# Kernel tuning notes

Measured on AMD Instinct MI355X. Metric: run time of the kernel, lower is better.

## Reference

```python
import jax, jax.numpy as jnp
import numpy as np

N, E, T = 6144, 98304, 32
D_IN, D, D_FF, H, OUT = 128, 256, 256, 4, 2
DH = D // H
EPS = 1e-5


def setup_inputs() -> dict:
    key = jax.random.key(0)
    ks = jax.random.split(key, 24)
    s = 0.05
    inp = {
        "x": jax.random.normal(ks[0], (N, D_IN), jnp.float32),
        "edge_index": jax.random.randint(ks[1], (2, E), 0, N, jnp.int64 if jax.config.jax_enable_x64 else jnp.int32),
        "timesteps": jnp.sort(jax.random.randint(ks[2], (N,), 0, T)),
        "lin_l_w": jax.random.normal(ks[3], (D, D_IN), jnp.float32) * s,
        "lin_l_b": jnp.zeros((D,), jnp.float32),
        "lin_r_w": jax.random.normal(ks[4], (D, D_IN), jnp.float32) * s,
        "bn_gamma": jnp.ones((D,), jnp.float32),
        "bn_beta": jnp.zeros((D,), jnp.float32),
        "in_proj_w": jax.random.normal(ks[5], (2, 3 * D, D), jnp.float32) * s,
        "in_proj_b": jnp.zeros((2, 3 * D), jnp.float32),
        "out_w": jax.random.normal(ks[6], (2, D, D), jnp.float32) * s,
        "out_b": jnp.zeros((2, D), jnp.float32),
        "ff1_w": jax.random.normal(ks[7], (2, D_FF, D), jnp.float32) * s,
        "ff1_b": jnp.zeros((2, D_FF), jnp.float32),
        "ff2_w": jax.random.normal(ks[8], (2, D, D_FF), jnp.float32) * s,
        "ff2_b": jnp.zeros((2, D), jnp.float32),
        "ln1_g": jnp.ones((2, D), jnp.float32),
        "ln1_b": jnp.zeros((2, D), jnp.float32),
        "ln2_g": jnp.ones((2, D), jnp.float32),
        "ln2_b": jnp.zeros((2, D), jnp.float32),
        "cls_w": jax.random.normal(ks[9], (OUT, D), jnp.float32) * s,
        "cls_b": jnp.zeros((OUT,), jnp.float32),
    }
    return inp


def _layernorm(h, g, b):
    mu = jnp.mean(h, -1, keepdims=True)
    v = jnp.var(h, -1, keepdims=True)
    return (h - mu) * jax.lax.rsqrt(v + EPS) * g + b


def _forward(x, edge_index, timesteps, lin_l_w, lin_l_b, lin_r_w, bn_gamma, bn_beta,
             in_proj_w, in_proj_b, out_w, out_b, ff1_w, ff1_b, ff2_w, ff2_b,
             ln1_g, ln1_b, ln2_g, ln2_b, cls_w, cls_b):
    # SAGEConv (mean aggregation): out = lin_l(mean_{j->i} x_j) + lin_r(x_i)
    src, dst = edge_index[0], edge_index[1]
    agg = jax.ops.segment_sum(x[src], dst, num_segments=N)
    cnt = jax.ops.segment_sum(jnp.ones((E,), x.dtype), dst, num_segments=N)
    agg = agg / jnp.maximum(cnt, 1.0)[:, None]
    h = agg @ lin_l_w.T + lin_l_b + x @ lin_r_w.T

    # BatchNorm1d (training batch stats) + ReLU
    mu = jnp.mean(h, 0)
    var = jnp.var(h, 0)
    h = (h - mu) * jax.lax.rsqrt(var + EPS) * bn_gamma + bn_beta
    h = jax.nn.relu(h)

    # Per-timestep transformer == full attention with block-diagonal mask
    mask = timesteps[:, None] == timesteps[None, :]  # [N, N]
    neg = jnp.finfo(h.dtype).min

    for l in range(2):
        # self-attention (post-norm TransformerEncoderLayer)
        qkv = h @ in_proj_w[l].T + in_proj_b[l]             # [N, 3D]
        q, k, v = jnp.split(qkv, 3, axis=-1)
        q = q.reshape(N, H, DH).transpose(1, 0, 2)          # [H, N, DH]
        k = k.reshape(N, H, DH).transpose(1, 0, 2)
        v = v.reshape(N, H, DH).transpose(1, 0, 2)
        scores = jnp.einsum('hnd,hmd->hnm', q, k) / jnp.sqrt(jnp.asarray(DH, h.dtype))
        scores = jnp.where(mask[None], scores, neg)
        attn = jax.nn.softmax(scores, axis=-1)
        o = jnp.einsum('hnm,hmd->hnd', attn, v).transpose(1, 0, 2).reshape(N, D)
        o = o @ out_w[l].T + out_b[l]
        h = _layernorm(h + o, ln1_g[l], ln1_b[l])
        # FFN
        f = jax.nn.relu(h @ ff1_w[l].T + ff1_b[l]) @ ff2_w[l].T + ff2_b[l]
        h = _layernorm(h + f, ln2_g[l], ln2_b[l])

    return h @ cls_w.T + cls_b  # [N, OUT]


def reference(x, edge_index, timesteps, lin_l_w, lin_l_b, lin_r_w, bn_gamma, bn_beta,
              in_proj_w, in_proj_b, out_w, out_b, ff1_w, ff1_b, ff2_w, ff2_b,
              ln1_g, ln1_b, ln2_g, ln2_b, cls_w, cls_b):
    return _forward(x, edge_index, timesteps, lin_l_w, lin_l_b, lin_r_w, bn_gamma, bn_beta,
                    in_proj_w, in_proj_b, out_w, out_b, ff1_w, ff1_b, ff2_w, ff2_b,
                    ln1_g, ln1_b, ln2_g, ln2_b, cls_w, cls_b)
```

## Files before the change

kernel.cpp:

```cpp
#include <hip/hip_runtime.h>

#define NN   6144
#define EE   98304
#define DIN  128
#define DD   256
#define TT   32
#define NH   4
#define ATTN_Z 6
#define WROWS 3328

typedef __attribute__((ext_vector_type(8))) short short8;
typedef __attribute__((ext_vector_type(4))) float f32x4;
typedef unsigned short u16;

__device__ __forceinline__ float bf2f(u16 u) {
    return __uint_as_float(((unsigned)u) << 16);
}
__device__ __forceinline__ u16 f2bf(float f) {
    unsigned u = __float_as_uint(f);
    return (u16)((u + 0x7fffu + ((u >> 16) & 1u)) >> 16);
}
__device__ __forceinline__ unsigned pk2(float a, float b) {
    return (unsigned)f2bf(a) | ((unsigned)f2bf(b) << 16);
}

__global__ void aml_hist_k(const int* __restrict__ ei, int* __restrict__ deg) {
    int e = blockIdx.x * 256 + threadIdx.x;
    if (e < EE) atomicAdd(&deg[ei[EE + e]], 1);
}

__global__ void aml_scan_k(const int* __restrict__ deg, int* __restrict__ rowptr,
                           int* __restrict__ cursor) {
    int t = threadIdx.x;
    int base = t * 24;
    int loc[24];
    int s = 0;
    #pragma unroll
    for (int j = 0; j < 24; ++j) { loc[j] = s; s += deg[base + j]; }
    __shared__ int part[256];
    part[t] = s;
    __syncthreads();
    for (int o = 1; o < 256; o <<= 1) {
        int v = (t >= o) ? part[t - o] : 0;
        __syncthreads();
        part[t] += v;
        __syncthreads();
    }
    int off = (t > 0) ? part[t - 1] : 0;
    #pragma unroll
    for (int j = 0; j < 24; ++j) {
        rowptr[base + j] = off + loc[j];
        cursor[base + j] = off + loc[j];
    }
    if (t == 255) rowptr[NN] = part[255];
}

__global__ void aml_scatter2_k(const int* __restrict__ ei, int* __restrict__ cursor,
                               int* __restrict__ eid) {
    int e = blockIdx.x * 256 + threadIdx.x;
    if (e >= EE) return;
    int slot = atomicAdd(&cursor[ei[EE + e]], 1);
    eid[slot] = ei[e];
}

__global__ void aml_gather_k(const float* __restrict__ x, const int* __restrict__ rowptr,
                             const int* __restrict__ eid, u16* __restrict__ ac) {
    int node = blockIdx.x * 4 + (threadIdx.x >> 6);
    int lane = threadIdx.x & 63;
    int p0 = rowptr[node], p1 = rowptr[node + 1];
    float ax = 0.f, ay = 0.f;
    int j = p0;
    for (; j + 1 < p1; j += 2) {
        int s0 = eid[j], s1 = eid[j + 1];
        float2 v0 = *(const float2*)(x + (size_t)s0 * DIN + lane * 2);
        float2 v1 = *(const float2*)(x + (size_t)s1 * DIN + lane * 2);
        ax += v0.x + v1.x; ay += v0.y + v1.y;
    }
    if (j < p1) {
        float2 v = *(const float2*)(x + (size_t)eid[j] * DIN + lane * 2);
        ax += v.x; ay += v.y;
    }
    float inv = 1.0f / fmaxf((float)(p1 - p0), 1.0f);
    float2 xr = *(const float2*)(x + (size_t)node * DIN + lane * 2);
    *(unsigned*)(ac + (size_t)node * DD + lane * 2) = pk2(ax * inv, ay * inv);
    *(unsigned*)(ac + (size_t)node * DD + DIN + lane * 2) = pk2(xr.x, xr.y);
}

__global__ void aml_prep_k(const float* __restrict__ lin_l_w, const float* __restrict__ lin_r_w,
                           const float* __restrict__ inp_w, const float* __restrict__ out_w,
                           const float* __restrict__ ff1_w, const float* __restrict__ ff2_w,
                           const int* __restrict__ ts, u16* __restrict__ wb,
                           int* __restrict__ offs) {
    int r = blockIdx.x;
    if (r == WROWS) {
        int t = threadIdx.x;
        if (t <= TT) {
            int lo = 0, hi = NN;
            while (lo < hi) { int mid = (lo + hi) >> 1; if (ts[mid] < t) lo = mid + 1; else hi = mid; }
            offs[t] = lo;
        }
        return;
    }
    int k = threadIdx.x;
    float v;
    if (r < 256) {
        v = (k < DIN) ? lin_l_w[r * DIN + k] : lin_r_w[r * DIN + (k - DIN)];
    } else {
        int r2 = r - 256;
        int l = r2 / 1536, r3 = r2 % 1536;
        const float* src; int rr;
        if (r3 < 768)       { src = inp_w + (size_t)l * 768 * DD; rr = r3; }
        else if (r3 < 1024) { src = out_w + (size_t)l * DD * DD;  rr = r3 - 768; }
        else if (r3 < 1280) { src = ff1_w + (size_t)l * DD * DD;  rr = r3 - 1024; }
        else                { src = ff2_w + (size_t)l * DD * DD;  rr = r3 - 1280; }
        v = src[(size_t)rr * DD + k];
    }
    wb[(size_t)r * DD + k] = f2bf(v);
}

template <int RELU, int AF32, int CF32, int BNSTAT>
__global__ __launch_bounds__(256)
void aml_gemm_k(const void* __restrict__ A, const u16* __restrict__ Wb,
                const float* __restrict__ bias, void* __restrict__ C, int M,
                float* __restrict__ stats) {
    __shared__ __align__(16) unsigned char lds[65536];
    const int t = threadIdx.x;
    const int brow = blockIdx.x * 64;
    const int bcol = blockIdx.y * 64;

    const u16* srcW = Wb + (size_t)bcol * 256;
    #pragma unroll
    for (int p = 0; p < 8; ++p) {
        int c = t + p * 256;
        int row = c >> 5;
        int colb = (c & 31) * 16;
        int dst = row * 512 + (colb ^ ((row & 7) << 4));
        if (AF32) {
            const float* sA = (const float*)A + (size_t)(brow + row) * 256 + (c & 31) * 8;
            float4 a0 = *(const float4*)sA;
            float4 a1 = *(const float4*)(sA + 4);
            uint4 pa = { pk2(a0.x, a0.y), pk2(a0.z, a0.w), pk2(a1.x, a1.y), pk2(a1.z, a1.w) };
            *(uint4*)(lds + dst) = pa;
        } else {
            const u16* sA = (const u16*)A + (size_t)(brow + row) * 256 + (c & 31) * 8;
            *(uint4*)(lds + dst) = *(const uint4*)sA;
        }
        *(uint4*)(lds + 32768 + dst) = *(const uint4*)(srcW + (size_t)row * 256 + (c & 31) * 8);
    }
    __syncthreads();

    const int wave = t >> 6, lane = t & 63;
    const int lrow = lane & 15, lk = lane >> 4;
    const int arow = wave * 16 + lrow;
    f32x4 acc[4] = {};
    #pragma unroll
    for (int ks = 0; ks < 8; ++ks) {
        int kbyte = ks * 64 + lk * 16;
        short8 af = *(const short8*)(lds + arow * 512 + (kbyte ^ ((arow & 7) << 4)));
        #pragma unroll
        for (int ct = 0; ct < 4; ++ct) {
            int wrow = ct * 16 + lrow;
            short8 bf = *(const short8*)(lds + 32768 + wrow * 512 + (kbyte ^ ((wrow & 7) << 4)));
            acc[ct] = __builtin_amdgcn_mfma_f32_16x16x32_bf16(af, bf, acc[ct], 0, 0, 0);
        }
    }

    #pragma unroll
    for (int ct = 0; ct < 4; ++ct) {
        int col = bcol + ct * 16 + lrow;
        float bv = bias[col];
        float s = 0.f, q = 0.f;
        #pragma unroll
        for (int r = 0; r < 4; ++r) {
            int grow = brow + wave * 16 + lk * 4 + r;
            float v = acc[ct][r] + bv;
            if (RELU) v = fmaxf(v, 0.0f);
            if (CF32) ((float*)C)[(size_t)grow * M + col] = v;
            else      ((u16*)C)[(size_t)grow * M + col] = f2bf(v);
            if (BNSTAT) { s += v; q += v * v; }
        }
        if (BNSTAT) {
            s += __shfl_xor(s, 16); s += __shfl_xor(s, 32);
            q += __shfl_xor(q, 16); q += __shfl_xor(q, 32);
            if (lk == 0) {
                atomicAdd(&stats[col], s);
                atomicAdd(&stats[DD + col], q);
            }
        }
    }
}

__global__ void aml_bn_apply_k(float* __restrict__ h, const float* __restrict__ stats,
                               const float* __restrict__ g, const float* __restrict__ b) {
    int idx = blockIdx.x * 256 + threadIdx.x;
    int d = idx & (DD - 1);
    float mu = stats[d] * (1.0f / NN);
    float var = stats[DD + d] * (1.0f / NN) - mu * mu;
    float v = (h[idx] - mu) * rsqrtf(var + 1e-5f) * g[d] + b[d];
    h[idx] = fmaxf(v, 0.0f);
}

template <int CLS>
__global__ __launch_bounds__(256)
void aml_mega_k(const u16* __restrict__ A, const u16* __restrict__ Wb,
                const float* __restrict__ bias, float* __restrict__ h,
                const float* __restrict__ g, const float* __restrict__ bv,
                const float* __restrict__ cls_w, const float* __restrict__ cls_b,
                float* __restrict__ out) {
    __shared__ __align__(16) unsigned char lds[65536];
    const int t = threadIdx.x;
    const int brow = blockIdx.x * 64;

    #pragma unroll
    for (int p = 0; p < 8; ++p) {
        int c = t + p * 256;
        int row = c >> 5;
        int colb = (c & 31) * 16;
        int dst = row * 512 + (colb ^ ((row & 7) << 4));
        const u16* sA = A + (size_t)(brow + row) * 256 + (c & 31) * 8;
        *(uint4*)(lds + dst) = *(const uint4*)sA;
    }
    #pragma unroll
    for (int p = 0; p < 8; ++p) {
        int c = t + p * 256;
        int row = c >> 5;
        int colb = (c & 31) * 16;
        int dst = 32768 + row * 512 + (colb ^ ((row & 7) << 4));
        *(uint4*)(lds + dst) = *(const uint4*)(Wb + (size_t)row * 256 + (c & 31) * 8);
    }
    __syncthreads();

    const int wave = t >> 6, lane = t & 63;
    const int lrow = lane & 15, lk = lane >> 4;
    const int arow = wave * 16 + lrow;

    short8 af[8];
    #pragma unroll
    for (int ks = 0; ks < 8; ++ks) {
        int kbyte = ks * 64 + lk * 16;
        af[ks] = *(const short8*)(lds + arow * 512 + (kbyte ^ ((arow & 7) << 4)));
    }

    f32x4 acc[4][4] = {};
    for (int cT = 0; cT < 4; ++cT) {
        if (cT) {
            __syncthreads();
            #pragma unroll
            for (int p = 0; p < 8; ++p) {
                int c = t + p * 256;
                int row = c >> 5;
                int colb = (c & 31) * 16;
                int dst = 32768 + row * 512 + (colb ^ ((row & 7) << 4));
                *(uint4*)(lds + dst) = *(const uint4*)(Wb + (size_t)(cT * 64 + row) * 256 + (c & 31) * 8);
            }
            __syncthreads();
        }
        #pragma unroll
        for (int ks = 0; ks < 8; ++ks) {
            int kbyte = ks * 64 + lk * 16;
            #pragma unroll
            for (int ct = 0; ct < 4; ++ct) {
                int wrow = ct * 16 + lrow;
                short8 bf = *(const short8*)(lds + 32768 + wrow * 512 + (kbyte ^ ((wrow & 7) << 4)));
                acc[cT][ct] = __builtin_amdgcn_mfma_f32_16x16x32_bf16(af[ks], bf, acc[cT][ct], 0, 0, 0);
            }
        }
    }

    float s[4] = {}, q[4] = {};
    #pragma unroll
    for (int cT = 0; cT < 4; ++cT) {
        #pragma unroll
        for (int ct = 0; ct < 4; ++ct) {
            int col = cT * 64 + ct * 16 + lrow;
            float bvv = bias[col];
            #pragma unroll
            for (int r = 0; r < 4; ++r) {
                int grow = brow + wave * 16 + lk * 4 + r;
                float v = acc[cT][ct][r] + bvv + h[(size_t)grow * DD + col];
                acc[cT][ct][r] = v;
                s[r] += v; q[r] += v * v;
            }
        }
    }
    #pragma unroll
    for (int off = 1; off < 16; off <<= 1) {
        #pragma unroll
        for (int r = 0; r < 4; ++r) {
            s[r] += __shfl_xor(s[r], off);
            q[r] += __shfl_xor(q[r], off);
        }
    }
    float mu[4], iv[4];
    #pragma unroll
    for (int r = 0; r < 4; ++r) {
        mu[r] = s[r] * (1.0f / DD);
        iv[r] = rsqrtf(q[r] * (1.0f / DD) - mu[r] * mu[r] + 1e-5f);
    }
    float c0[4] = {}, c1[4] = {};
    #pragma unroll
    for (int cT = 0; cT < 4; ++cT) {
        #pragma unroll
        for (int ct = 0; ct < 4; ++ct) {
            int col = cT * 64 + ct * 16 + lrow;
            float gv = g[col], bb = bv[col];
            float w0 = CLS ? cls_w[col] : 0.f;
            float w1 = CLS ? cls_w[DD + col] : 0.f;
            #pragma unroll
            for (int r = 0; r < 4; ++r) {
                int grow = brow + wave * 16 + lk * 4 + r;
                float v = (acc[cT][ct][r] - mu[r]) * iv[r] * gv + bb;
                h[(size_t)grow * DD + col] = v;
                if (CLS) { c0[r] += v * w0; c1[r] += v * w1; }
            }
        }
    }
    if (CLS) {
        #pragma unroll
        for (int off = 1; off < 16; off <<= 1) {
            #pragma unroll
            for (int r = 0; r < 4; ++r) {
                c0[r] += __shfl_xor(c0[r], off);
                c1[r] += __shfl_xor(c1[r], off);
            }
        }
        if (lrow == 0) {
            float cb0 = cls_b[0], cb1 = cls_b[1];
            #pragma unroll
            for (int r = 0; r < 4; ++r) {
                int grow = brow + wave * 16 + lk * 4 + r;
                out[grow * 2]     = c0[r] + cb0;
                out[grow * 2 + 1] = c1[r] + cb1;
            }
        }
    }
}

__global__ __launch_bounds__(256)
void aml_attn_k(const u16* __restrict__ qkv, const int* __restrict__ offs,
                u16* __restrict__ o) {
    int tb = blockIdx.x, head = blockIdx.y, z = blockIdx.z;
    int start = offs[tb], end = offs[tb + 1];
    int S = end - start;
    if (S <= z * 64) return;
    int t = threadIdx.x, wave = t >> 6, lane = t & 63;
    int lq = lane & 15, lk = lane >> 4;
    int qoff = head * 64;

    __shared__ __align__(16) unsigned char Kl[8192];
    __shared__ __align__(16) unsigned char Vt[8192];
    __shared__ __align__(16) unsigned char Pl[4][2048];
    __shared__ float Ol[4][16][65];

    int qi = start + z * 64 + wave * 16 + lq;
    int qic = min(qi, end - 1);
    const u16* qp = qkv + (size_t)qic * 768 + qoff + lk * 8;
    short8 qf[2];
    qf[0] = *(const short8*)qp;
    qf[1] = *(const short8*)(qp + 32);

    float m = -1e30f, l = 0.f;
    f32x4 acc[4] = {};

    int ntile = (S + 63) >> 6;
    for (int tile = 0; tile < ntile; ++tile) {
        int jcnt = S - tile * 64; if (jcnt > 64) jcnt = 64;
        {
            int j = t >> 2, d0 = (t & 3) * 16;
            unsigned char* krow = Kl + j * 128;
            if (j < jcnt) {
                const u16* kp = qkv + (size_t)(start + tile * 64 + j) * 768 + 256 + qoff + d0;
                *(uint4*)(krow + ((d0 * 2) ^ ((j & 7) << 4))) = *(const uint4*)kp;
                *(uint4*)(krow + ((d0 * 2 + 16) ^ ((j & 7) << 4))) = *(const uint4*)(kp + 8);
                const u16* vp = kp + 256;
                #pragma unroll
                for (int i = 0; i < 16; ++i) {
                    int d = d0 + i;
                    *(u16*)(Vt + d * 128 + ((j * 2) ^ ((d & 7) << 4))) = vp[i];
                }
            } else {
                uint4 zz = { 0, 0, 0, 0 };
                *(uint4*)(krow + ((d0 * 2) ^ ((j & 7) << 4))) = zz;
                *(uint4*)(krow + ((d0 * 2 + 16) ^ ((j & 7) << 4))) = zz;
                #pragma unroll
                for (int i = 0; i < 16; ++i) {
                    int d = d0 + i;
                    *(u16*)(Vt + d * 128 + ((j * 2) ^ ((d & 7) << 4))) = 0;
                }
            }
        }
        __syncthreads();

        f32x4 sv[4];
        #pragma unroll
        for (int kt = 0; kt < 4; ++kt) {
            int kr = kt * 16 + lq;
            f32x4 s = {};
            #pragma unroll
            for (int ks = 0; ks < 2; ++ks) {
                short8 kf = *(const short8*)(Kl + kr * 128 + ((ks * 64 + lk * 16) ^ ((kr & 7) << 4)));
                s = __builtin_amdgcn_mfma_f32_16x16x32_bf16(kf, qf[ks], s, 0, 0, 0);
            }
            sv[kt] = s;
        }
        float pm = -1e30f;
        #pragma unroll
        for (int kt = 0; kt < 4; ++kt) {
            #pragma unroll
            for (int r = 0; r < 4; ++r) {
                int kk = tile * 64 + kt * 16 + lk * 4 + r;
                float s = (kk < S) ? sv[kt][r] * 0.125f : -1e30f;
                sv[kt][r] = s;
                pm = fmaxf(pm, s);
            }
        }
        pm = fmaxf(pm, __shfl_xor(pm, 16));
        pm = fmaxf(pm, __shfl_xor(pm, 32));
        float mn = fmaxf(m, pm);
        float corr = __expf(m - mn);
        m = mn;
        float ps = 0.f;
        #pragma unroll
        for (int kt = 0; kt < 4; ++kt) {
            #pragma unroll
            for (int r = 0; r < 4; ++r) {
                float p = __expf(sv[kt][r] - mn);
                sv[kt][r] = p;
                ps += p;
            }
            uint2 w = { pk2(sv[kt][0], sv[kt][1]), pk2(sv[kt][2], sv[kt][3]) };
            *(uint2*)(Pl[wave] + lq * 128 + ((kt * 32 + lk * 8) ^ ((lq & 7) << 4))) = w;
        }
        ps += __shfl_xor(ps, 16);
        ps += __shfl_xor(ps, 32);
        l = l * corr + ps;
        #pragma unroll
        for (int dt = 0; dt < 4; ++dt) {
            #pragma unroll
            for (int r = 0; r < 4; ++r) acc[dt][r] *= corr;
        }
        #pragma unroll
        for (int ks = 0; ks < 2; ++ks) {
            short8 pf = *(const short8*)(Pl[wave] + lq * 128 + ((ks * 64 + lk * 16) ^ ((lq & 7) << 4)));
            #pragma unroll
            for (int dt = 0; dt < 4; ++dt) {
                int dr = dt * 16 + lq;
                short8 vf = *(const short8*)(Vt + dr * 128 + ((ks * 64 + lk * 16) ^ ((dr & 7) << 4)));
                acc[dt] = __builtin_amdgcn_mfma_f32_16x16x32_bf16(vf, pf, acc[dt], 0, 0, 0);
            }
        }
        __syncthreads();
    }

    float linv = 1.0f / l;
    #pragma unroll
    for (int dt = 0; dt < 4; ++dt) {
        #pragma unroll
        for (int r = 0; r < 4; ++r)
            Ol[wave][lq][dt * 16 + lk * 4 + r] = acc[dt][r] * linv;
    }
    int q2 = lane >> 2, c2 = lane & 3;
    int qg = start + z * 64 + wave * 16 + q2;
    if (qg < end) {
        u16* op = o + (size_t)qg * DD + qoff + c2 * 16;
        const float* sp = &Ol[wave][q2][c2 * 16];
        #pragma unroll
        for (int i = 0; i < 8; ++i)
            ((unsigned*)op)[i] = pk2(sp[2 * i], sp[2 * i + 1]);
    }
}

extern "C" void kernel_launch(void* const* d_in, const int* in_sizes, int n_in,
                              void* d_out, int out_size, void* d_ws, size_t ws_size,
                              hipStream_t stream) {
    const float* x       = (const float*)d_in[0];
    const int*   ei      = (const int*)d_in[1];
    const int*   ts      = (const int*)d_in[2];
    const float* lin_l_w = (const float*)d_in[3];
    const float* lin_l_b = (const float*)d_in[4];
    const float* lin_r_w = (const float*)d_in[5];
    const float* bn_g    = (const float*)d_in[6];
    const float* bn_b    = (const float*)d_in[7];
    const float* inp_w   = (const float*)d_in[8];
    const float* inp_b   = (const float*)d_in[9];
    const float* out_w   = (const float*)d_in[10];
    const float* out_b   = (const float*)d_in[11];
    const float* ff1_w   = (const float*)d_in[12];
    const float* ff1_b   = (const float*)d_in[13];
    const float* ff2_w   = (const float*)d_in[14];
    const float* ff2_b   = (const float*)d_in[15];
    const float* ln1_g   = (const float*)d_in[16];
    const float* ln1_b   = (const float*)d_in[17];
    const float* ln2_g   = (const float*)d_in[18];
    const float* ln2_b   = (const float*)d_in[19];
    const float* cls_w   = (const float*)d_in[20];
    const float* cls_b   = (const float*)d_in[21];

    float* ws     = (float*)d_ws;
    float* stats  = ws;
    int*   deg    = (int*)(stats + 512);
    int*   rowptr = deg + NN;
    int*   cursor = rowptr + NN + 4;
    int*   eid    = cursor + NN;
    int*   offs   = eid + EE;
    u16*   wb     = (u16*)(offs + 64);
    float* h      = (float*)(wb + (size_t)WROWS * 256);
    u16*   qkv    = (u16*)(h + (size_t)NN * DD);
    u16*   t1     = qkv + (size_t)NN * 768;
    u16*   ac     = qkv;

    const u16* wb_cat = wb;
    const u16* wb_inp[2] = { wb + (size_t)(256) * 256,        wb + (size_t)(256 + 1536) * 256 };
    const u16* wb_out[2] = { wb + (size_t)(256 + 768) * 256,  wb + (size_t)(256 + 1536 + 768) * 256 };
    const u16* wb_ff1[2] = { wb + (size_t)(256 + 1024) * 256, wb + (size_t)(256 + 1536 + 1024) * 256 };
    const u16* wb_ff2[2] = { wb + (size_t)(256 + 1280) * 256, wb + (size_t)(256 + 1536 + 1280) * 256 };

    hipMemsetAsync(stats, 0, 512 * sizeof(float) + NN * sizeof(int), stream);

    aml_hist_k<<<EE / 256, 256, 0, stream>>>(ei, deg);
    aml_scan_k<<<1, 256, 0, stream>>>(deg, rowptr, cursor);
    aml_scatter2_k<<<EE / 256, 256, 0, stream>>>(ei, cursor, eid);
    aml_gather_k<<<NN / 4, 256, 0, stream>>>(x, rowptr, eid, ac);
    aml_prep_k<<<WROWS + 1, 256, 0, stream>>>(lin_l_w, lin_r_w, inp_w, out_w, ff1_w, ff2_w,
                                              ts, wb, offs);
    aml_gemm_k<0, 0, 1, 1><<<dim3(NN / 64, 4), 256, 0, stream>>>(ac, wb_cat, lin_l_b, h, DD, stats);
    aml_bn_apply_k<<<(NN * DD) / 256, 256, 0, stream>>>(h, stats, bn_g, bn_b);

    for (int l = 0; l < 2; ++l) {
        aml_gemm_k<0, 1, 0, 0><<<dim3(NN / 64, 12), 256, 0, stream>>>(h, wb_inp[l],
                                                                      inp_b + (size_t)l * 768,
                                                                      qkv, 768, nullptr);
        aml_attn_k<<<dim3(TT, NH, ATTN_Z), 256, 0, stream>>>(qkv, offs, t1);
        aml_mega_k<0><<<NN / 64, 256, 0, stream>>>(t1, wb_out[l], out_b + (size_t)l * DD, h,
                                                   ln1_g + (size_t)l * DD, ln1_b + (size_t)l * DD,
                                                   nullptr, nullptr, nullptr);
        aml_gemm_k<1, 1, 0, 0><<<dim3(NN / 64, 4), 256, 0, stream>>>(h, wb_ff1[l],
                                                                     ff1_b + (size_t)l * DD,
                                                                     t1, DD, nullptr);
        if (l == 0)
            aml_mega_k<0><<<NN / 64, 256, 0, stream>>>(t1, wb_ff2[l], ff2_b + (size_t)l * DD, h,
                                                       ln2_g + (size_t)l * DD, ln2_b + (size_t)l * DD,
                                                       nullptr, nullptr, nullptr);
        else
            aml_mega_k<1><<<NN / 64, 256, 0, stream>>>(t1, wb_ff2[l], ff2_b + (size_t)l * DD, h,
                                                       ln2_g + (size_t)l * DD, ln2_b + (size_t)l * DD,
                                                       cls_w, cls_b, (float*)d_out);
    }
}
```

Measured before the change: 164.6 us.

## Process two query chunks per attention block to reuse staged K/V tiles

Each attention block now covers 128 queries as two 64-query chunks instead of 64, halving the grid z dimension and reusing each staged K/V tile and K fragments across both chunks. The V transpose into LDS is rewritten to use vectorized 16-byte global loads with packed 32-bit LDS stores instead of scalar u16 traffic. The PV MFMA operand order is swapped so the output is laid out query-per-column, which removes the Ol LDS staging buffer but makes the final stores scattered 2-byte writes and requires shuffles for the per-row correction factors. Fewer blocks and higher register use may reduce parallelism for short timestep segments.

```diff
diff --git a/kernel.cpp b/kernel.cpp
--- a/kernel.cpp
+++ b/kernel.cpp
@@ -6,7 +6,7 @@
 #define DD   256
 #define TT   32
 #define NH   4
-#define ATTN_Z 6
+#define ATTN_Z 3
 #define WROWS 3328
 
 typedef __attribute__((ext_vector_type(8))) short short8;
@@ -342,7 +342,7 @@
     int tb = blockIdx.x, head = blockIdx.y, z = blockIdx.z;
     int start = offs[tb], end = offs[tb + 1];
     int S = end - start;
-    if (S <= z * 64) return;
+    if (S <= z * 128) return;
     int t = threadIdx.x, wave = t >> 6, lane = t & 63;
     int lq = lane & 15, lk = lane >> 4;
     int qoff = head * 64;
@@ -350,17 +350,19 @@
     __shared__ __align__(16) unsigned char Kl[8192];
     __shared__ __align__(16) unsigned char Vt[8192];
     __shared__ __align__(16) unsigned char Pl[4][2048];
-    __shared__ float Ol[4][16][65];
-
-    int qi = start + z * 64 + wave * 16 + lq;
-    int qic = min(qi, end - 1);
-    const u16* qp = qkv + (size_t)qic * 768 + qoff + lk * 8;
-    short8 qf[2];
-    qf[0] = *(const short8*)qp;
-    qf[1] = *(const short8*)(qp + 32);
-
-    float m = -1e30f, l = 0.f;
-    f32x4 acc[4] = {};
+
+    short8 qf[2][2];
+    float m[2], l[2];
+    f32x4 acc[2][4] = {};
+    #pragma unroll
+    for (int c = 0; c < 2; ++c) {
+        int qi = start + z * 128 + c * 64 + wave * 16 + lq;
+        int qic = min(qi, end - 1);
+        const u16* qp = qkv + (size_t)qic * 768 + qoff + lk * 8;
+        qf[c][0] = *(const short8*)qp;
+        qf[c][1] = *(const short8*)(qp + 32);
+        m[c] = -1e30f; l[c] = 0.f;
+    }
 
     int ntile = (S + 63) >> 6;
     for (int tile = 0; tile < ntile; ++tile) {
@@ -372,101 +374,115 @@
                 const u16* kp = qkv + (size_t)(start + tile * 64 + j) * 768 + 256 + qoff + d0;
                 *(uint4*)(krow + ((d0 * 2) ^ ((j & 7) << 4))) = *(const uint4*)kp;
                 *(uint4*)(krow + ((d0 * 2 + 16) ^ ((j & 7) << 4))) = *(const uint4*)(kp + 8);
-                const u16* vp = kp + 256;
-                #pragma unroll
-                for (int i = 0; i < 16; ++i) {
-                    int d = d0 + i;
-                    *(u16*)(Vt + d * 128 + ((j * 2) ^ ((d & 7) << 4))) = vp[i];
-                }
             } else {
                 uint4 zz = { 0, 0, 0, 0 };
                 *(uint4*)(krow + ((d0 * 2) ^ ((j & 7) << 4))) = zz;
                 *(uint4*)(krow + ((d0 * 2 + 16) ^ ((j & 7) << 4))) = zz;
-                #pragma unroll
-                for (int i = 0; i < 16; ++i) {
-                    int d = d0 + i;
-                    *(u16*)(Vt + d * 128 + ((j * 2) ^ ((d & 7) << 4))) = 0;
-                }
+            }
+        }
+        {
+            int j0 = (t & 31) * 2, d0v = (t >> 5) * 8;
+            const u16* vbase = qkv + (size_t)(start + tile * 64) * 768 + 512 + qoff + d0v;
+            uint4 va = { 0, 0, 0, 0 }, vb = { 0, 0, 0, 0 };
+            if (j0 < jcnt)     va = *(const uint4*)(vbase + (size_t)j0 * 768);
+            if (j0 + 1 < jcnt) vb = *(const uint4*)(vbase + (size_t)(j0 + 1) * 768);
+            const u16* pa = (const u16*)&va;
+            const u16* pb = (const u16*)&vb;
+            #pragma unroll
+            for (int i = 0; i < 8; ++i) {
+                int d = d0v + i;
+                unsigned w = (unsigned)pa[i] | ((unsigned)pb[i] << 16);
+                *(unsigned*)(Vt + d * 128 + ((j0 * 2) ^ ((d & 7) << 4))) = w;
             }
         }
         __syncthreads();
 
-        f32x4 sv[4];
+        short8 kf[4][2];
         #pragma unroll
         for (int kt = 0; kt < 4; ++kt) {
             int kr = kt * 16 + lq;
-            f32x4 s = {};
+            #pragma unroll
+            for (int ks = 0; ks < 2; ++ks)
+                kf[kt][ks] = *(const short8*)(Kl + kr * 128 + ((ks * 64 + lk * 16) ^ ((kr & 7) << 4)));
+        }
+
+        #pragma unroll
+        for (int c = 0; c < 2; ++c) {
+            if (z * 128 + c * 64 >= S) break;
+            f32x4 sv[4];
+            #pragma unroll
+            for (int kt = 0; kt < 4; ++kt) {
+                f32x4 s = {};
+                s = __builtin_amdgcn_mfma_f32_16x16x32_bf16(kf[kt][0], qf[c][0], s, 0, 0, 0);
+                s = __builtin_amdgcn_mfma_f32_16x16x32_bf16(kf[kt][1], qf[c][1], s, 0, 0, 0);
+                sv[kt] = s;
+            }
+            float pm = -1e30f;
+            #pragma unroll
+            for (int kt = 0; kt < 4; ++kt) {
+                #pragma unroll
+                for (int r = 0; r < 4; ++r) {
+                    int kk = tile * 64 + kt * 16 + lk * 4 + r;
+                    float s = (kk < S) ? sv[kt][r] * 0.125f : -1e30f;
+                    sv[kt][r] = s;
+                    pm = fmaxf(pm, s);
+                }
+            }
+            pm = fmaxf(pm, __shfl_xor(pm, 16));
+            pm = fmaxf(pm, __shfl_xor(pm, 32));
+            float mn = fmaxf(m[c], pm);
+            float corr = __expf(m[c] - mn);
+            m[c] = mn;
+            float ps = 0.f;
+            #pragma unroll
+            for (int kt = 0; kt < 4; ++kt) {
+                #pragma unroll
+                for (int r = 0; r < 4; ++r) {
+                    float p = __expf(sv[kt][r] - mn);
+                    sv[kt][r] = p;
+                    ps += p;
+                }
+                uint2 w = { pk2(sv[kt][0], sv[kt][1]), pk2(sv[kt][2], sv[kt][3]) };
+                *(uint2*)(Pl[wave] + lq * 128 + ((kt * 32 + lk * 8) ^ ((lq & 7) << 4))) = w;
+            }
+            ps += __shfl_xor(ps, 16);
+            ps += __shfl_xor(ps, 32);
+            l[c] = l[c] * corr + ps;
+            float cr[4];
+            #pragma unroll
+            for (int r = 0; r < 4; ++r) cr[r] = __shfl(corr, lk * 4 + r);
+            #pragma unroll
+            for (int dt = 0; dt < 4; ++dt)
+                #pragma unroll
+                for (int r = 0; r < 4; ++r) acc[c][dt][r] *= cr[r];
             #pragma unroll
             for (int ks = 0; ks < 2; ++ks) {
-                short8 kf = *(const short8*)(Kl + kr * 128 + ((ks * 64 + lk * 16) ^ ((kr & 7) << 4)));
-                s = __builtin_amdgcn_mfma_f32_16x16x32_bf16(kf, qf[ks], s, 0, 0, 0);
-            }
-            sv[kt] = s;
-        }
-        float pm = -1e30f;
-        #pragma unroll
-        for (int kt = 0; kt < 4; ++kt) {
-            #pragma unroll
-            for (int r = 0; r < 4; ++r) {
-                int kk = tile * 64 + kt * 16 + lk * 4 + r;
-                float s = (kk < S) ? sv[kt][r] * 0.125f : -1e30f;
-                sv[kt][r] = s;
-                pm = fmaxf(pm, s);
-            }
-        }
-        pm = fmaxf(pm, __shfl_xor(pm, 16));
-        pm = fmaxf(pm, __shfl_xor(pm, 32));
-        float mn = fmaxf(m, pm);
-        float corr = __expf(m - mn);
-        m = mn;
-        float ps = 0.f;
-        #pragma unroll
-        for (int kt = 0; kt < 4; ++kt) {
-            #pragma unroll
-            for (int r = 0; r < 4; ++r) {
-                float p = __expf(sv[kt][r] - mn);
-                sv[kt][r] = p;
-                ps += p;
-            }
-            uint2 w = { pk2(sv[kt][0], sv[kt][1]), pk2(sv[kt][2], sv[kt][3]) };
-            *(uint2*)(Pl[wave] + lq * 128 + ((kt * 32 + lk * 8) ^ ((lq & 7) << 4))) = w;
-        }
-        ps += __shfl_xor(ps, 16);
-        ps += __shfl_xor(ps, 32);
-        l = l * corr + ps;
-        #pragma unroll
-        for (int dt = 0; dt < 4; ++dt) {
-            #pragma unroll
-            for (int r = 0; r < 4; ++r) acc[dt][r] *= corr;
-        }
-        #pragma unroll
-        for (int ks = 0; ks < 2; ++ks) {
-            short8 pf = *(const short8*)(Pl[wave] + lq * 128 + ((ks * 64 + lk * 16) ^ ((lq & 7) << 4)));
-            #pragma unroll
-            for (int dt = 0; dt < 4; ++dt) {
-                int dr = dt * 16 + lq;
-                short8 vf = *(const short8*)(Vt + dr * 128 + ((ks * 64 + lk * 16) ^ ((dr & 7) << 4)));
-                acc[dt] = __builtin_amdgcn_mfma_f32_16x16x32_bf16(vf, pf, acc[dt], 0, 0, 0);
+                short8 pf = *(const short8*)(Pl[wave] + lq * 128 + ((ks * 64 + lk * 16) ^ ((lq & 7) << 4)));
+                #pragma unroll
+                for (int dt = 0; dt < 4; ++dt) {
+                    int dr = dt * 16 + lq;
+                    short8 vf = *(const short8*)(Vt + dr * 128 + ((ks * 64 + lk * 16) ^ ((dr & 7) << 4)));
+                    acc[c][dt] = __builtin_amdgcn_mfma_f32_16x16x32_bf16(pf, vf, acc[c][dt], 0, 0, 0);
+                }
             }
         }
         __syncthreads();
     }
 
-    float linv = 1.0f / l;
-    #pragma unroll
-    for (int dt = 0; dt < 4; ++dt) {
-        #pragma unroll
-        for (int r = 0; r < 4; ++r)
-            Ol[wave][lq][dt * 16 + lk * 4 + r] = acc[dt][r] * linv;
-    }
-    int q2 = lane >> 2, c2 = lane & 3;
-    int qg = start + z * 64 + wave * 16 + q2;
-    if (qg < end) {
-        u16* op = o + (size_t)qg * DD + qoff + c2 * 16;
-        const float* sp = &Ol[wave][q2][c2 * 16];
-        #pragma unroll
-        for (int i = 0; i < 8; ++i)
-            ((unsigned*)op)[i] = pk2(sp[2 * i], sp[2 * i + 1]);
+    #pragma unroll
+    for (int c = 0; c < 2; ++c) {
+        if (z * 128 + c * 64 >= S) break;
+        #pragma unroll
+        for (int r = 0; r < 4; ++r) {
+            float linv = 1.0f / __shfl(l[c], lk * 4 + r);
+            int qg = start + z * 128 + c * 64 + wave * 16 + lk * 4 + r;
+            if (qg < end) {
+                u16* op = o + (size_t)qg * DD + qoff + lq;
+                #pragma unroll
+                for (int dt = 0; dt < 4; ++dt)
+                    op[dt * 16] = f2bf(acc[c][dt][r] * linv);
+            }
+        }
     }
 }
 
```

New measurement: 173.7 us. +5.5%, slower.

## Fuse BN-apply into first QKV GEMM and retile mega kernel to 16-row blocks

Applied to the files above, without the earlier changes.

Removes the standalone batch-norm apply kernel by applying BN+ReLU while loading A in the layer-0 QKV GEMM. The blockIdx.y==0 blocks write the normalized activations to a new h2 buffer used downstream. The residual+LayerNorm mega kernel is restructured so each block handles 16 rows with four waves splitting the 256 output columns. Weights are streamed in K chunks, and row statistics and classifier sums are reduced across waves through shared memory. This gives four times as many blocks for better occupancy and parallelism, at the cost of each block re-reading the full weight matrix, plus extra syncs and a larger workspace.

```diff
diff --git a/kernel.cpp b/kernel.cpp
--- a/kernel.cpp
+++ b/kernel.cpp
@@ -22,6 +22,11 @@
 }
 __device__ __forceinline__ unsigned pk2(float a, float b) {
     return (unsigned)f2bf(a) | ((unsigned)f2bf(b) << 16);
+}
+__device__ __forceinline__ float bnrelu(float v, float s, float q, float g, float b) {
+    float mu = s * (1.0f / NN);
+    float var = q * (1.0f / NN) - mu * mu;
+    return fmaxf((v - mu) * rsqrtf(var + 1e-5f) * g + b, 0.0f);
 }
 
 __global__ void aml_hist_k(const int* __restrict__ ei, int* __restrict__ deg) {
@@ -118,11 +123,12 @@
     wb[(size_t)r * DD + k] = f2bf(v);
 }
 
-template <int RELU, int AF32, int CF32, int BNSTAT>
+template <int RELU, int AF32, int CF32, int BNSTAT, int BNAPPLY>
 __global__ __launch_bounds__(256)
 void aml_gemm_k(const void* __restrict__ A, const u16* __restrict__ Wb,
                 const float* __restrict__ bias, void* __restrict__ C, int M,
-                float* __restrict__ stats) {
+                float* __restrict__ stats, const float* __restrict__ bng,
+                const float* __restrict__ bnb, float* __restrict__ h2) {
     __shared__ __align__(16) unsigned char lds[65536];
     const int t = threadIdx.x;
     const int brow = blockIdx.x * 64;
@@ -139,6 +145,28 @@
             const float* sA = (const float*)A + (size_t)(brow + row) * 256 + (c & 31) * 8;
             float4 a0 = *(const float4*)sA;
             float4 a1 = *(const float4*)(sA + 4);
+            if (BNAPPLY) {
+                int d0 = (c & 31) * 8;
+                float4 s0 = *(const float4*)(stats + d0);
+                float4 s1 = *(const float4*)(stats + d0 + 4);
+                float4 q0 = *(const float4*)(stats + DD + d0);
+                float4 q1 = *(const float4*)(stats + DD + d0 + 4);
+                float4 g0 = *(const float4*)(bng + d0), g1 = *(const float4*)(bng + d0 + 4);
+                float4 b0 = *(const float4*)(bnb + d0), b1 = *(const float4*)(bnb + d0 + 4);
+                a0.x = bnrelu(a0.x, s0.x, q0.x, g0.x, b0.x);
+                a0.y = bnrelu(a0.y, s0.y, q0.y, g0.y, b0.y);
+                a0.z = bnrelu(a0.z, s0.z, q0.z, g0.z, b0.z);
+                a0.w = bnrelu(a0.w, s0.w, q0.w, g0.w, b0.w);
+                a1.x = bnrelu(a1.x, s1.x, q1.x, g1.x, b1.x);
+                a1.y = bnrelu(a1.y, s1.y, q1.y, g1.y, b1.y);
+                a1.z = bnrelu(a1.z, s1.z, q1.z, g1.z, b1.z);
+                a1.w = bnrelu(a1.w, s1.w, q1.w, g1.w, b1.w);
+                if (blockIdx.y == 0) {
+                    float* hp = h2 + (size_t)(brow + row) * 256 + d0;
+                    *(float4*)hp = a0;
+                    *(float4*)(hp + 4) = a1;
+                }
+            }
             uint4 pa = { pk2(a0.x, a0.y), pk2(a0.z, a0.w), pk2(a1.x, a1.y), pk2(a1.z, a1.w) };
             *(uint4*)(lds + dst) = pa;
         } else {
@@ -190,16 +218,6 @@
     }
 }
 
-__global__ void aml_bn_apply_k(float* __restrict__ h, const float* __restrict__ stats,
-                               const float* __restrict__ g, const float* __restrict__ b) {
-    int idx = blockIdx.x * 256 + threadIdx.x;
-    int d = idx & (DD - 1);
-    float mu = stats[d] * (1.0f / NN);
-    float var = stats[DD + d] * (1.0f / NN) - mu * mu;
-    float v = (h[idx] - mu) * rsqrtf(var + 1e-5f) * g[d] + b[d];
-    h[idx] = fmaxf(v, 0.0f);
-}
-
 template <int CLS>
 __global__ __launch_bounds__(256)
 void aml_mega_k(const u16* __restrict__ A, const u16* __restrict__ Wb,
@@ -207,112 +225,107 @@
                 const float* __restrict__ g, const float* __restrict__ bv,
                 const float* __restrict__ cls_w, const float* __restrict__ cls_b,
                 float* __restrict__ out) {
-    __shared__ __align__(16) unsigned char lds[65536];
+    __shared__ __align__(16) unsigned char Al[8192];
+    __shared__ __align__(16) unsigned char Wl[32768];
+    __shared__ float reds[4][16], redq[4][16];
+    __shared__ float redc[2][4][16];
     const int t = threadIdx.x;
-    const int brow = blockIdx.x * 64;
-
-    #pragma unroll
-    for (int p = 0; p < 8; ++p) {
+    const int brow = blockIdx.x * 16;
+    const int wave = t >> 6, lane = t & 63;
+    const int lrow = lane & 15, lk = lane >> 4;
+    const int wcol = wave * 64;
+
+    #pragma unroll
+    for (int p = 0; p < 2; ++p) {
         int c = t + p * 256;
         int row = c >> 5;
-        int colb = (c & 31) * 16;
-        int dst = row * 512 + (colb ^ ((row & 7) << 4));
-        const u16* sA = A + (size_t)(brow + row) * 256 + (c & 31) * 8;
-        *(uint4*)(lds + dst) = *(const uint4*)sA;
-    }
-    #pragma unroll
-    for (int p = 0; p < 8; ++p) {
-        int c = t + p * 256;
-        int row = c >> 5;
-        int colb = (c & 31) * 16;
-        int dst = 32768 + row * 512 + (colb ^ ((row & 7) << 4));
-        *(uint4*)(lds + dst) = *(const uint4*)(Wb + (size_t)row * 256 + (c & 31) * 8);
+        int c8 = c & 31;
+        const u16* sA = A + (size_t)(brow + row) * 256 + c8 * 8;
+        *(uint4*)(Al + row * 512 + ((c8 * 16) ^ ((row & 7) << 4))) = *(const uint4*)sA;
+    }
+
+    short8 af[8];
+    f32x4 acc[4] = {};
+    for (int kc = 0; kc < 4; ++kc) {
+        if (kc) __syncthreads();
+        #pragma unroll
+        for (int p = 0; p < 8; ++p) {
+            int c = t + p * 256;
+            int row = c >> 3, sub = c & 7;
+            *(uint4*)(Wl + row * 128 + ((sub * 16) ^ ((row & 7) << 4))) =
+                *(const uint4*)(Wb + (size_t)row * 256 + kc * 64 + sub * 8);
+        }
+        __syncthreads();
+        if (kc == 0) {
+            #pragma unroll
+            for (int ks = 0; ks < 8; ++ks) {
+                int kbyte = ks * 64 + lk * 16;
+                af[ks] = *(const short8*)(Al + lrow * 512 + (kbyte ^ ((lrow & 7) << 4)));
+            }
+        }
+        #pragma unroll
+        for (int s = 0; s < 2; ++s) {
+            int kb = s * 64 + lk * 16;
+            #pragma unroll
+            for (int ct = 0; ct < 4; ++ct) {
+                int wrow = wcol + ct * 16 + lrow;
+                short8 bf = *(const short8*)(Wl + wrow * 128 + (kb ^ ((wrow & 7) << 4)));
+                acc[ct] = __builtin_amdgcn_mfma_f32_16x16x32_bf16(af[kc * 2 + s], bf, acc[ct], 0, 0, 0);
+            }
+        }
+    }
+
+    float s4[4] = {}, q4[4] = {};
+    #pragma unroll
+    for (int ct = 0; ct < 4; ++ct) {
+        int col = wcol + ct * 16 + lrow;
+        float bvv = bias[col];
+        #pragma unroll
+        for (int r = 0; r < 4; ++r) {
+            int grow = brow + lk * 4 + r;
+            float v = acc[ct][r] + bvv + h[(size_t)grow * DD + col];
+            acc[ct][r] = v;
+            s4[r] += v; q4[r] += v * v;
+        }
+    }
+    #pragma unroll
+    for (int off = 1; off < 16; off <<= 1) {
+        #pragma unroll
+        for (int r = 0; r < 4; ++r) {
+            s4[r] += __shfl_xor(s4[r], off);
+            q4[r] += __shfl_xor(q4[r], off);
+        }
+    }
+    if (lrow == 0) {
+        #pragma unroll
+        for (int r = 0; r < 4; ++r) {
+            reds[wave][lk * 4 + r] = s4[r];
+            redq[wave][lk * 4 + r] = q4[r];
+        }
     }
     __syncthreads();
-
-    const int wave = t >> 6, lane = t & 63;
-    const int lrow = lane & 15, lk = lane >> 4;
-    const int arow = wave * 16 + lrow;
-
-    short8 af[8];
-    #pragma unroll
-    for (int ks = 0; ks < 8; ++ks) {
-        int kbyte = ks * 64 + lk * 16;
-        af[ks] = *(const short8*)(lds + arow * 512 + (kbyte ^ ((arow & 7) << 4)));
-    }
-
-    f32x4 acc[4][4] = {};
-    for (int cT = 0; cT < 4; ++cT) {
-        if (cT) {
-            __syncthreads();
-            #pragma unroll
-            for (int p = 0; p < 8; ++p) {
-                int c = t + p * 256;
-                int row = c >> 5;
-                int colb = (c & 31) * 16;
-                int dst = 32768 + row * 512 + (colb ^ ((row & 7) << 4));
-                *(uint4*)(lds + dst) = *(const uint4*)(Wb + (size_t)(cT * 64 + row) * 256 + (c & 31) * 8);
-            }
-            __syncthreads();
-        }
-        #pragma unroll
-        for (int ks = 0; ks < 8; ++ks) {
-            int kbyte = ks * 64 + lk * 16;
-            #pragma unroll
-            for (int ct = 0; ct < 4; ++ct) {
-                int wrow = ct * 16 + lrow;
-                short8 bf = *(const short8*)(lds + 32768 + wrow * 512 + (kbyte ^ ((wrow & 7) << 4)));
-                acc[cT][ct] = __builtin_amdgcn_mfma_f32_16x16x32_bf16(af[ks], bf, acc[cT][ct], 0, 0, 0);
-            }
-        }
-    }
-
-    float s[4] = {}, q[4] = {};
-    #pragma unroll
-    for (int cT = 0; cT < 4; ++cT) {
-        #pragma unroll
-        for (int ct = 0; ct < 4; ++ct) {
-            int col = cT * 64 + ct * 16 + lrow;
-            float bvv = bias[col];
-            #pragma unroll
-            for (int r = 0; r < 4; ++r) {
-                int grow = brow + wave * 16 + lk * 4 + r;
-                float v = acc[cT][ct][r] + bvv + h[(size_t)grow * DD + col];
-                acc[cT][ct][r] = v;
-                s[r] += v; q[r] += v * v;
-            }
-        }
-    }
-    #pragma unroll
-    for (int off = 1; off < 16; off <<= 1) {
+    float mu[4], iv[4];
+    #pragma unroll
+    for (int r = 0; r < 4; ++r) {
+        int rr = lk * 4 + r;
+        float S = reds[0][rr] + reds[1][rr] + reds[2][rr] + reds[3][rr];
+        float Q = redq[0][rr] + redq[1][rr] + redq[2][rr] + redq[3][rr];
+        mu[r] = S * (1.0f / DD);
+        iv[r] = rsqrtf(Q * (1.0f / DD) - mu[r] * mu[r] + 1e-5f);
+    }
+    float c0[4] = {}, c1[4] = {};
+    #pragma unroll
+    for (int ct = 0; ct < 4; ++ct) {
+        int col = wcol + ct * 16 + lrow;
+        float gv = g[col], bb = bv[col];
+        float w0 = CLS ? cls_w[col] : 0.f;
+        float w1 = CLS ? cls_w[DD + col] : 0.f;
         #pragma unroll
         for (int r = 0; r < 4; ++r) {
-            s[r] += __shfl_xor(s[r], off);
-            q[r] += __shfl_xor(q[r], off);
-        }
-    }
-    float mu[4], iv[4];
-    #pragma unroll
-    for (int r = 0; r < 4; ++r) {
-        mu[r] = s[r] * (1.0f / DD);
-        iv[r] = rsqrtf(q[r] * (1.0f / DD) - mu[r] * mu[r] + 1e-5f);
-    }
-    float c0[4] = {}, c1[4] = {};
-    #pragma unroll
-    for (int cT = 0; cT < 4; ++cT) {
-        #pragma unroll
-        for (int ct = 0; ct < 4; ++ct) {
-            int col = cT * 64 + ct * 16 + lrow;
-            float gv = g[col], bb = bv[col];
-            float w0 = CLS ? cls_w[col] : 0.f;
-            float w1 = CLS ? cls_w[DD + col] : 0.f;
-            #pragma unroll
-            for (int r = 0; r < 4; ++r) {
-                int grow = brow + wave * 16 + lk * 4 + r;
-                float v = (acc[cT][ct][r] - mu[r]) * iv[r] * gv + bb;
-                h[(size_t)grow * DD + col] = v;
-                if (CLS) { c0[r] += v * w0; c1[r] += v * w1; }
-            }
+            int grow = brow + lk * 4 + r;
+            float v = (acc[ct][r] - mu[r]) * iv[r] * gv + bb;
+            h[(size_t)grow * DD + col] = v;
+            if (CLS) { c0[r] += v * w0; c1[r] += v * w1; }
         }
     }
     if (CLS) {
@@ -325,12 +338,22 @@
             }
         }
         if (lrow == 0) {
+            #pragma unroll
+            for (int r = 0; r < 4; ++r) {
+                redc[0][wave][lk * 4 + r] = c0[r];
+                redc[1][wave][lk * 4 + r] = c1[r];
+            }
+        }
+        __syncthreads();
+        if (wave == 0 && lrow == 0) {
             float cb0 = cls_b[0], cb1 = cls_b[1];
             #pragma unroll
             for (int r = 0; r < 4; ++r) {
-                int grow = brow + wave * 16 + lk * 4 + r;
-                out[grow * 2]     = c0[r] + cb0;
-                out[grow * 2 + 1] = c1[r] + cb1;
+                int rr = lk * 4 + r;
+                float o0 = redc[0][0][rr] + redc[0][1][rr] + redc[0][2][rr] + redc[0][3][rr];
+                float o1 = redc[1][0][rr] + redc[1][1][rr] + redc[1][2][rr] + redc[1][3][rr];
+                out[(brow + rr) * 2]     = o0 + cb0;
+                out[(brow + rr) * 2 + 1] = o1 + cb1;
             }
         }
     }
@@ -505,7 +528,8 @@
     int*   offs   = eid + EE;
     u16*   wb     = (u16*)(offs + 64);
     float* h      = (float*)(wb + (size_t)WROWS * 256);
-    u16*   qkv    = (u16*)(h + (size_t)NN * DD);
+    float* h2     = h + (size_t)NN * DD;
+    u16*   qkv    = (u16*)(h2 + (size_t)NN * DD);
     u16*   t1     = qkv + (size_t)NN * 768;
     u16*   ac     = qkv;
 
@@ -523,27 +547,28 @@
     aml_gather_k<<<NN / 4, 256, 0, stream>>>(x, rowptr, eid, ac);
     aml_prep_k<<<WROWS + 1, 256, 0, stream>>>(lin_l_w, lin_r_w, inp_w, out_w, ff1_w, ff2_w,
                                               ts, wb, offs);
-    aml_gemm_k<0, 0, 1, 1><<<dim3(NN / 64, 4), 256, 0, stream>>>(ac, wb_cat, lin_l_b, h, DD, stats);
-    aml_bn_apply_k<<<(NN * DD) / 256, 256, 0, stream>>>(h, stats, bn_g, bn_b);
+    aml_gemm_k<0, 0, 1, 1, 0><<<dim3(NN / 64, 4), 256, 0, stream>>>(
+        ac, wb_cat, lin_l_b, h, DD, stats, nullptr, nullptr, nullptr);
 
     for (int l = 0; l < 2; ++l) {
-        aml_gemm_k<0, 1, 0, 0><<<dim3(NN / 64, 12), 256, 0, stream>>>(h, wb_inp[l],
-                                                                      inp_b + (size_t)l * 768,
-                                                                      qkv, 768, nullptr);
+        if (l == 0)
+            aml_gemm_k<0, 1, 0, 0, 1><<<dim3(NN / 64, 12), 256, 0, stream>>>(
+                h, wb_inp[0], inp_b, qkv, 768, stats, bn_g, bn_b, h2);
+        else
+            aml_gemm_k<0, 1, 0, 0, 0><<<dim3(NN / 64, 12), 256, 0, stream>>>(
+                h2, wb_inp[1], inp_b + 768, qkv, 768, nullptr, nullptr, nullptr, nullptr);
         aml_attn_k<<<dim3(TT, NH, ATTN_Z), 256, 0, stream>>>(qkv, offs, t1);
-        aml_mega_k<0><<<NN / 64, 256, 0, stream>>>(t1, wb_out[l], out_b + (size_t)l * DD, h,
+        aml_mega_k<0><<<NN / 16, 256, 0, stream>>>(t1, wb_out[l], out_b + (size_t)l * DD, h2,
                                                    ln1_g + (size_t)l * DD, ln1_b + (size_t)l * DD,
                                                    nullptr, nullptr, nullptr);
-        aml_gemm_k<1, 1, 0, 0><<<dim3(NN / 64, 4), 256, 0, stream>>>(h, wb_ff1[l],
-                                                                     ff1_b + (size_t)l * DD,
-                                                                     t1, DD, nullptr);
+        aml_gemm_k<1, 1, 0, 0, 0><<<dim3(NN / 64, 4), 256, 0, stream>>>(
+            h2, wb_ff1[l], ff1_b + (size_t)l * DD, t1, DD, nullptr, nullptr, nullptr, nullptr);
         if (l == 0)
-            aml_mega_k<0><<<NN / 64, 256, 0, stream>>>(t1, wb_ff2[l], ff2_b + (size_t)l * DD, h,
-                                                       ln2_g + (size_t)l * DD, ln2_b + (size_t)l * DD,
-                                                       nullptr, nullptr, nullptr);
+            aml_mega_k<0><<<NN / 16, 256, 0, stream>>>(t1, wb_ff2[0], ff2_b, h2,
+                                                       ln2_g, ln2_b, nullptr, nullptr, nullptr);
         else
-            aml_mega_k<1><<<NN / 64, 256, 0, stream>>>(t1, wb_ff2[l], ff2_b + (size_t)l * DD, h,
-                                                       ln2_g + (size_t)l * DD, ln2_b + (size_t)l * DD,
+            aml_mega_k<1><<<NN / 16, 256, 0, stream>>>(t1, wb_ff2[1], ff2_b + DD, h2,
+                                                       ln2_g + DD, ln2_b + DD,
                                                        cls_w, cls_b, (float*)d_out);
     }
 }
```

Result: no change. 162.5 us (-1.3%).
